# Kernel tuning notes

Measured on AMD Instinct MI355X. Metric: run time of the kernel, lower is better.

The kernel has to match this reference:

```python
import jax, jax.numpy as jnp
import numpy as np

IN_DIM, N_WIN, OUT_DIM = 128, 64, 128


def setup_inputs() -> dict:
    key = jax.random.key(0)
    kx, kw, kb = jax.random.split(key, 3)
    k = 1.0 / (IN_DIM * N_WIN)
    bound = float(np.sqrt(k))
    x = jax.random.normal(kx, (IN_DIM, 8192), dtype=jnp.float32)
    weight = jax.random.uniform(kw, (IN_DIM, N_WIN, OUT_DIM), dtype=jnp.float32,
                                minval=-bound, maxval=bound)
    bias = jax.random.uniform(kb, (OUT_DIM,), dtype=jnp.float32,
                              minval=-bound, maxval=bound)
    return {"x": x, "weight": weight, "bias": bias}


def reference(x, weight, bias):
    # x: (inDim, N); weight: (inDim, nWin, outDim); bias: (outDim,)
    # Original: TRFs[n,i,w,o] = x[n,i]*W[i,w,o] + bias[o], then sum over i.
    # Fused: out[n,w,o] = sum_i x[n,i]*W[i,w,o] + inDim*bias[o]
    in_dim = weight.shape[0]
    out = jnp.einsum('in,iwo->nwo', x, weight)
    out = out + in_dim * bias  # bias added before sum over inDim in original
    return out
```

## Files before the change

kernel.cpp:

```cpp
#include <hip/hip_runtime.h>
#include <hip/hip_bf16.h>
#include <stdint.h>

#define K_DIM 128
#define N_X   8192
#define N_WO  8192
#define OUT_TOTAL (8192UL * 64UL * 128UL)
#define CHUNKS_PER_PANEL 131072

typedef __attribute__((ext_vector_type(8))) short short8;
typedef __attribute__((ext_vector_type(4))) float f32x4;

__device__ inline unsigned short f2bf(float f) {
    union { float f; unsigned u; } v; v.f = f;
    unsigned u = v.u;
    u += 0x7fffu + ((u >> 16) & 1u);
    return (unsigned short)(u >> 16);
}

__global__ __launch_bounds__(256) void prep_frag2(const float* __restrict__ X,
                                                  const float* __restrict__ W,
                                                  uint4* __restrict__ Q) {
    int c  = blockIdx.x * 256 + threadIdx.x;
    int cc = c & (CHUNKS_PER_PANEL - 1);
    const float* P = (c >= CHUNKS_PER_PANEL) ? W : X;
    int l  = cc & 63;
    int ks = (cc >> 6) & 3;
    int t  = cc >> 8;
    int m  = t * 16 + (l & 15);
    int k0 = ks * 32 + ((l >> 4) << 3);
    const float* p = P + (size_t)k0 * N_X + m;
    unsigned short h[8];
#pragma unroll
    for (int j = 0; j < 8; ++j) h[j] = f2bf(p[(size_t)j * N_X]);
    uint4 q;
    q.x = (unsigned)h[0] | ((unsigned)h[1] << 16);
    q.y = (unsigned)h[2] | ((unsigned)h[3] << 16);
    q.z = (unsigned)h[4] | ((unsigned)h[5] << 16);
    q.w = (unsigned)h[6] | ((unsigned)h[7] << 16);
    Q[c] = q;
}

__global__ __launch_bounds__(512, 2) void gemm_sweep(const short8* __restrict__ A,
                                                     const short8* __restrict__ B,
                                                     const float* __restrict__ bias,
                                                     float* __restrict__ out) {
    int bid = blockIdx.x;
    int swz = (bid & 7) * 32 + (bid >> 3);
    int n0  = swz * 32;

    int tid  = threadIdx.x;
    int lane = tid & 63;
    int w    = tid >> 6;

    int tA = swz * 2;
    short8 xf[2][4];
#pragma unroll
    for (int i = 0; i < 2; ++i)
#pragma unroll
        for (int ks = 0; ks < 4; ++ks)
            xf[i][ks] = A[((tA + i) * 4 + ks) * 64 + lane];

    int cl = lane & 15, rg = (lane >> 4) << 2;

    f32x4 bvs[4];
#pragma unroll
    for (int j = 0; j < 4; ++j) {
        const f32x4 bv = *(const f32x4*)(bias + ((((w * 4 + j) & 7) << 4) + rg));
        bvs[j].x = 128.0f * bv.x;  bvs[j].y = 128.0f * bv.y;
        bvs[j].z = 128.0f * bv.z;  bvs[j].w = 128.0f * bv.w;
    }

    float* out0 = out + (size_t)n0 * N_WO;
    float* out1 = out0 + 16 * N_WO;

#pragma unroll 2
    for (int it = 0; it < 16; ++it) {
        int tj0 = it * 32 + w * 4;
        short8 wf[4][4];
#pragma unroll
        for (int j = 0; j < 4; ++j)
#pragma unroll
            for (int ks = 0; ks < 4; ++ks)
                wf[j][ks] = B[((tj0 + j) * 4 + ks) * 64 + lane];

        f32x4 acc[2][4] = {};
#pragma unroll
        for (int ks = 0; ks < 4; ++ks)
#pragma unroll
            for (int i = 0; i < 2; ++i)
#pragma unroll
                for (int j = 0; j < 4; ++j)
                    acc[i][j] = __builtin_amdgcn_mfma_f32_16x16x32_bf16(
                        wf[j][ks], xf[i][ks], acc[i][j], 0, 0, 0);

        float* po0 = out0 + (size_t)cl * N_WO;
        float* po1 = out1 + (size_t)cl * N_WO;
#pragma unroll
        for (int j = 0; j < 4; ++j) {
            int wo = (tj0 + j) * 16 + rg;
            f32x4 v0 = acc[0][j], v1 = acc[1][j];
            v0.x += bvs[j].x; v0.y += bvs[j].y; v0.z += bvs[j].z; v0.w += bvs[j].w;
            v1.x += bvs[j].x; v1.y += bvs[j].y; v1.z += bvs[j].z; v1.w += bvs[j].w;
            *(f32x4*)(po0 + wo) = v0;
            *(f32x4*)(po1 + wo) = v1;
        }
    }
}

__global__ __launch_bounds__(256) void naive_kernel(const float* __restrict__ x,
                                                    const float* __restrict__ wgt,
                                                    const float* __restrict__ bias,
                                                    float* __restrict__ out) {
    size_t idx = (size_t)blockIdx.x * 256 + threadIdx.x;
    if (idx >= OUT_TOTAL) return;
    int n    = (int)(idx >> 13);
    int ncol = (int)(idx & 8191);
    float s = 0.f;
    for (int i = 0; i < K_DIM; ++i)
        s += x[(size_t)i * N_X + n] * wgt[(size_t)i * N_WO + ncol];
    out[idx] = s + 128.0f * bias[ncol & 127];
}

extern "C" void kernel_launch(void* const* d_in, const int* in_sizes, int n_in,
                              void* d_out, int out_size, void* d_ws, size_t ws_size,
                              hipStream_t stream) {
    const float* x    = (const float*)d_in[0];
    const float* wgt  = (const float*)d_in[1];
    const float* bias = (const float*)d_in[2];
    float* out = (float*)d_out;

    if (ws_size >= 4u * 1024u * 1024u) {
        uint4* wsA = (uint4*)d_ws;
        uint4* wsB = wsA + CHUNKS_PER_PANEL;
        prep_frag2<<<1024, 256, 0, stream>>>(x, wgt, wsA);
        gemm_sweep<<<256, 512, 0, stream>>>((const short8*)wsA, (const short8*)wsB,
                                            bias, out);
    } else {
        naive_kernel<<<(unsigned)((OUT_TOTAL + 255) / 256), 256, 0, stream>>>(
            x, wgt, bias, out);
    }
}
```

Before: 65.17 us.

## Convert x fragments inside GEMM and use nontemporal output stores

The prep kernel now converts only the weight panel to bf16 fragments. The GEMM kernel loads x directly from fp32 and packs its bf16 fragments in registers, which halves the prep work and removes the workspace round-trip for x. Output stores become nontemporal to reduce cache pollution from the large 256MB write stream. The cost is strided fp32 loads of x in the GEMM prologue, each redone by all 8 waves of a block.

```diff
diff --git a/kernel.cpp b/kernel.cpp
--- a/kernel.cpp
+++ b/kernel.cpp
@@ -18,18 +18,15 @@
     return (unsigned short)(u >> 16);
 }
 
-__global__ __launch_bounds__(256) void prep_frag2(const float* __restrict__ X,
-                                                  const float* __restrict__ W,
-                                                  uint4* __restrict__ Q) {
-    int c  = blockIdx.x * 256 + threadIdx.x;
-    int cc = c & (CHUNKS_PER_PANEL - 1);
-    const float* P = (c >= CHUNKS_PER_PANEL) ? W : X;
+__global__ __launch_bounds__(256) void prep_w(const float* __restrict__ W,
+                                              uint4* __restrict__ Q) {
+    int cc = blockIdx.x * 256 + threadIdx.x;
     int l  = cc & 63;
     int ks = (cc >> 6) & 3;
     int t  = cc >> 8;
     int m  = t * 16 + (l & 15);
     int k0 = ks * 32 + ((l >> 4) << 3);
-    const float* p = P + (size_t)k0 * N_X + m;
+    const float* p = W + (size_t)k0 * N_X + m;
     unsigned short h[8];
 #pragma unroll
     for (int j = 0; j < 8; ++j) h[j] = f2bf(p[(size_t)j * N_X]);
@@ -38,10 +35,10 @@
     q.y = (unsigned)h[2] | ((unsigned)h[3] << 16);
     q.z = (unsigned)h[4] | ((unsigned)h[5] << 16);
     q.w = (unsigned)h[6] | ((unsigned)h[7] << 16);
-    Q[c] = q;
+    Q[cc] = q;
 }
 
-__global__ __launch_bounds__(512, 2) void gemm_sweep(const short8* __restrict__ A,
+__global__ __launch_bounds__(512, 2) void gemm_sweep(const float* __restrict__ x,
                                                      const short8* __restrict__ B,
                                                      const float* __restrict__ bias,
                                                      float* __restrict__ out) {
@@ -52,16 +49,27 @@
     int tid  = threadIdx.x;
     int lane = tid & 63;
     int w    = tid >> 6;
+    int cl = lane & 15, rg = (lane >> 4) << 2;
 
-    int tA = swz * 2;
     short8 xf[2][4];
 #pragma unroll
-    for (int i = 0; i < 2; ++i)
+    for (int i = 0; i < 2; ++i) {
+        int m = (swz * 2 + i) * 16 + cl;
 #pragma unroll
-        for (int ks = 0; ks < 4; ++ks)
-            xf[i][ks] = A[((tA + i) * 4 + ks) * 64 + lane];
-
-    int cl = lane & 15, rg = (lane >> 4) << 2;
+        for (int ks = 0; ks < 4; ++ks) {
+            int k0 = ks * 32 + ((lane >> 4) << 3);
+            const float* p = x + (size_t)k0 * N_X + m;
+            unsigned short h[8];
+#pragma unroll
+            for (int j = 0; j < 8; ++j) h[j] = f2bf(p[(size_t)j * N_X]);
+            union { uint4 q; short8 s; } u;
+            u.q.x = (unsigned)h[0] | ((unsigned)h[1] << 16);
+            u.q.y = (unsigned)h[2] | ((unsigned)h[3] << 16);
+            u.q.z = (unsigned)h[4] | ((unsigned)h[5] << 16);
+            u.q.w = (unsigned)h[6] | ((unsigned)h[7] << 16);
+            xf[i][ks] = u.s;
+        }
+    }
 
     f32x4 bvs[4];
 #pragma unroll
@@ -82,7 +90,7 @@
         for (int j = 0; j < 4; ++j)
 #pragma unroll
             for (int ks = 0; ks < 4; ++ks)
-                wf[j][ks] = B[((tj0 + j) * 4 + ks) * 64 + lane];
+                wf[j][ks] = B[(size_t)((tj0 + j) * 4 + ks) * 64 + lane];
 
         f32x4 acc[2][4] = {};
 #pragma unroll
@@ -102,8 +110,8 @@
             f32x4 v0 = acc[0][j], v1 = acc[1][j];
             v0.x += bvs[j].x; v0.y += bvs[j].y; v0.z += bvs[j].z; v0.w += bvs[j].w;
             v1.x += bvs[j].x; v1.y += bvs[j].y; v1.z += bvs[j].z; v1.w += bvs[j].w;
-            *(f32x4*)(po0 + wo) = v0;
-            *(f32x4*)(po1 + wo) = v1;
+            __builtin_nontemporal_store(v0, (f32x4*)(po0 + wo));
+            __builtin_nontemporal_store(v1, (f32x4*)(po1 + wo));
         }
     }
 }
@@ -130,12 +138,10 @@
     const float* bias = (const float*)d_in[2];
     float* out = (float*)d_out;
 
-    if (ws_size >= 4u * 1024u * 1024u) {
-        uint4* wsA = (uint4*)d_ws;
-        uint4* wsB = wsA + CHUNKS_PER_PANEL;
-        prep_frag2<<<1024, 256, 0, stream>>>(x, wgt, wsA);
-        gemm_sweep<<<256, 512, 0, stream>>>((const short8*)wsA, (const short8*)wsB,
-                                            bias, out);
+    if (ws_size >= 2u * 1024u * 1024u) {
+        uint4* wsB = (uint4*)d_ws;
+        prep_w<<<512, 256, 0, stream>>>(wgt, wsB);
+        gemm_sweep<<<256, 512, 0, stream>>>(x, (const short8*)wsB, bias, out);
     } else {
         naive_kernel<<<(unsigned)((OUT_TOTAL + 255) / 256), 256, 0, stream>>>(
             x, wgt, bias, out);
```

Measured after the change: 97.23 us. 1.49x slower.

## Tile GEMM as 64-row slabs split in halves across XCD pairs

Applied to the files above, without the earlier changes.

Each block now covers 64 rows of the output (four 16-row X fragments) and only half of the column range, instead of 32 rows across all columns. The XCD-aware block mapping sends the two halves of a slab to paired XCDs. Each W fragment load now feeds twice as many MFMAs, cutting B traffic, and the two column halves of W are split across XCD L2 caches. The cost is more accumulator and fragment registers, which may pressure the two-blocks-per-CU occupancy, and the inner loop is no longer explicitly unrolled.

```diff
diff --git a/kernel.cpp b/kernel.cpp
--- a/kernel.cpp
+++ b/kernel.cpp
@@ -45,23 +45,24 @@
                                                      const short8* __restrict__ B,
                                                      const float* __restrict__ bias,
                                                      float* __restrict__ out) {
-    int bid = blockIdx.x;
-    int swz = (bid & 7) * 32 + (bid >> 3);
-    int n0  = swz * 32;
+    int bid  = blockIdx.x;
+    int xcd  = bid & 7;
+    int slot = bid >> 3;
+    int half = xcd & 1;
+    int slab = (xcd >> 1) * 32 + slot;
+    int n0   = slab * 64;
 
     int tid  = threadIdx.x;
     int lane = tid & 63;
     int w    = tid >> 6;
+    int cl = lane & 15, rg = (lane >> 4) << 2;
 
-    int tA = swz * 2;
-    short8 xf[2][4];
+    short8 xf[4][4];
 #pragma unroll
-    for (int i = 0; i < 2; ++i)
+    for (int i = 0; i < 4; ++i)
 #pragma unroll
         for (int ks = 0; ks < 4; ++ks)
-            xf[i][ks] = A[((tA + i) * 4 + ks) * 64 + lane];
-
-    int cl = lane & 15, rg = (lane >> 4) << 2;
+            xf[i][ks] = A[(size_t)((slab * 4 + i) * 4 + ks) * 64 + lane];
 
     f32x4 bvs[4];
 #pragma unroll
@@ -71,39 +72,42 @@
         bvs[j].z = 128.0f * bv.z;  bvs[j].w = 128.0f * bv.w;
     }
 
-    float* out0 = out + (size_t)n0 * N_WO;
-    float* out1 = out0 + 16 * N_WO;
+    float* po[4];
+#pragma unroll
+    for (int i = 0; i < 4; ++i)
+        po[i] = out + (size_t)(n0 + i * 16 + cl) * N_WO;
 
-#pragma unroll 2
-    for (int it = 0; it < 16; ++it) {
-        int tj0 = it * 32 + w * 4;
+    int tbase = half * 256;
+
+    for (int it = 0; it < 8; ++it) {
+        int tj0 = tbase + it * 32 + w * 4;
         short8 wf[4][4];
 #pragma unroll
         for (int j = 0; j < 4; ++j)
 #pragma unroll
             for (int ks = 0; ks < 4; ++ks)
-                wf[j][ks] = B[((tj0 + j) * 4 + ks) * 64 + lane];
+                wf[j][ks] = B[(size_t)((tj0 + j) * 4 + ks) * 64 + lane];
 
-        f32x4 acc[2][4] = {};
+        f32x4 acc[4][4] = {};
 #pragma unroll
         for (int ks = 0; ks < 4; ++ks)
 #pragma unroll
-            for (int i = 0; i < 2; ++i)
+            for (int i = 0; i < 4; ++i)
 #pragma unroll
                 for (int j = 0; j < 4; ++j)
                     acc[i][j] = __builtin_amdgcn_mfma_f32_16x16x32_bf16(
                         wf[j][ks], xf[i][ks], acc[i][j], 0, 0, 0);
 
-        float* po0 = out0 + (size_t)cl * N_WO;
-        float* po1 = out1 + (size_t)cl * N_WO;
 #pragma unroll
         for (int j = 0; j < 4; ++j) {
             int wo = (tj0 + j) * 16 + rg;
-            f32x4 v0 = acc[0][j], v1 = acc[1][j];
-            v0.x += bvs[j].x; v0.y += bvs[j].y; v0.z += bvs[j].z; v0.w += bvs[j].w;
-            v1.x += bvs[j].x; v1.y += bvs[j].y; v1.z += bvs[j].z; v1.w += bvs[j].w;
-            *(f32x4*)(po0 + wo) = v0;
-            *(f32x4*)(po1 + wo) = v1;
+#pragma unroll
+            for (int i = 0; i < 4; ++i) {
+                f32x4 v = acc[i][j];
+                v.x += bvs[j].x; v.y += bvs[j].y;
+                v.z += bvs[j].z; v.w += bvs[j].w;
+                *(f32x4*)(po[i] + wo) = v;
+            }
         }
     }
 }
@@ -134,8 +138,8 @@
         uint4* wsA = (uint4*)d_ws;
         uint4* wsB = wsA + CHUNKS_PER_PANEL;
         prep_frag2<<<1024, 256, 0, stream>>>(x, wgt, wsA);
-        gemm_sweep<<<256, 512, 0, stream>>>((const short8*)wsA, (const short8*)wsB,
-                                            bias, out);
+        gemm_sweep<<<256, 512, 0, stream>>>((const short8*)wsA,
+                                            (const short8*)wsB, bias, out);
     } else {
         naive_kernel<<<(unsigned)((OUT_TOTAL + 255) / 256), 256, 0, stream>>>(
             x, wgt, bias, out);
```

New measurement: 72.48 us. 1.11x slower.
